# Kernel optimization log

Measured on AMD Instinct MI355X. Metric: run time of the kernel, lower is better.

The kernel has to match this reference:

```python
import jax, jax.numpy as jnp
import numpy as np

N, IN_C, E = 50000, 512, 800000
H, C = 2, 64          # heads, per-head channels
HC = H * C            # 128
OUT_C = 2
B = 64                # number of graphs
EPS = 1e-5
NEG_SLOPE = 0.2


def gat_conv(x, src, dst, W, a_src, a_dst, bias):
    """PyG GATConv (concat=True, add_self_loops already included in src/dst)."""
    n = x.shape[0]
    h = (x @ W).reshape(n, H, C)                      # [N,H,C]
    alpha_src = (h * a_src[None]).sum(-1)             # [N,H]
    alpha_dst = (h * a_dst[None]).sum(-1)             # [N,H]
    e = jax.nn.leaky_relu(alpha_src[src] + alpha_dst[dst], NEG_SLOPE)  # [E,H]
    # segment softmax over incoming edges of each destination node
    m = jax.ops.segment_max(e, dst, num_segments=n)   # [N,H]
    ex = jnp.exp(e - m[dst])
    denom = jax.ops.segment_sum(ex, dst, num_segments=n)
    alpha = ex / denom[dst]                           # [E,H]
    msg = h[src] * alpha[:, :, None]                  # [E,H,C]
    out = jax.ops.segment_sum(msg, dst, num_segments=n)  # [N,H,C]
    return out.reshape(n, HC) + bias


def batch_norm(x, gamma, beta):
    # BatchNorm1d in training mode: batch statistics over the node dim
    mu = x.mean(0)
    var = x.var(0)
    return gamma * (x - mu) * jax.lax.rsqrt(var + EPS) + beta


def setup_inputs() -> dict:
    key = jax.random.key(0)
    ks = jax.random.split(key, 16)
    x = jax.random.normal(ks[0], (N, IN_C), dtype=jnp.float32)
    edge_index = jax.random.randint(ks[1], (2, E), 0, N, dtype=jnp.int64)
    batch = jnp.sort(jax.random.randint(ks[2], (N,), 0, B, dtype=jnp.int64))
    g = lambda k, sh, fan: jax.random.normal(k, sh, dtype=jnp.float32) * (1.0 / np.sqrt(fan))
    return {
        "x": x, "edge_index": edge_index, "batch": batch,
        "W1": g(ks[3], (IN_C, HC), IN_C),
        "att_src1": g(ks[4], (H, C), C), "att_dst1": g(ks[5], (H, C), C),
        "b1": jnp.zeros((HC,), jnp.float32),
        "gamma1": jnp.ones((HC,), jnp.float32), "beta1": jnp.zeros((HC,), jnp.float32),
        "W2": g(ks[6], (HC, HC), HC),
        "att_src2": g(ks[7], (H, C), C), "att_dst2": g(ks[8], (H, C), C),
        "b2": jnp.zeros((HC,), jnp.float32),
        "gamma2": jnp.ones((HC,), jnp.float32), "beta2": jnp.zeros((HC,), jnp.float32),
        "Wlin": g(ks[9], (HC, OUT_C), HC),
        "blin": jnp.zeros((OUT_C,), jnp.float32),
    }


def reference(x, edge_index, batch, W1, att_src1, att_dst1, b1, gamma1, beta1,
              W2, att_src2, att_dst2, b2, gamma2, beta2, Wlin, blin):
    n = x.shape[0]
    # GATConv adds self-loops by default
    loop = jnp.arange(n, dtype=edge_index.dtype)
    src = jnp.concatenate([edge_index[0], loop])
    dst = jnp.concatenate([edge_index[1], loop])

    h = gat_conv(x, src, dst, W1, att_src1, att_dst1, b1)
    h = jax.nn.relu(batch_norm(h, gamma1, beta1))
    h = gat_conv(h, src, dst, W2, att_src2, att_dst2, b2)
    h = jax.nn.relu(batch_norm(h, gamma2, beta2))

    # global mean pool over graphs
    sums = jax.ops.segment_sum(h, batch, num_segments=B)           # [B,HC]
    cnt = jax.ops.segment_sum(jnp.ones((n,), h.dtype), batch, num_segments=B)
    pooled = sums / jnp.maximum(cnt, 1.0)[:, None]
    return pooled @ Wlin + blin                                    # [B,OUT_C]
```

## Files before the change

### kernel.cpp

```cpp
#include <hip/hip_runtime.h>
#include <hip/hip_bf16.h>
#include <cstdint>
#include <cstddef>

#define NN      50000
#define IN_C    512
#define EE      800000
#define ETOT    850000
#define HH      2
#define CC      64
#define HC      128
#define BB      64
#define OUTC    2
#define NEG_SLOPE 0.2f
#define BN_EPS  1e-5f

#define NBLK_SCAN ((NN + 255) / 256)

#define NXCD     8
#define NPX      ((NN + NXCD - 1) / NXCD)
#define EDGES_PER_SLOT 2048
#define NSLOT    ((ETOT + EDGES_PER_SLOT - 1) / EDGES_PER_SLOT)

typedef __bf16 bf16x8 __attribute__((ext_vector_type(8)));
typedef float  f32x4  __attribute__((ext_vector_type(4)));

__device__ __forceinline__ unsigned f2bf(float f) {
    __bf16 b = (__bf16)f;
    return (unsigned)__builtin_bit_cast(unsigned short, b);
}

__device__ __forceinline__ void gload_lds16(const float* g, float* l) {
    __builtin_amdgcn_global_load_lds(
        (const __attribute__((address_space(1))) unsigned*)g,
        (__attribute__((address_space(3))) unsigned*)l,
        16, 0, 0);
}

__global__ __launch_bounds__(256) void deg_kernel(const int* __restrict__ ei, int* __restrict__ deg)
{
    const int xcd  = blockIdx.x & (NXCD - 1);
    const int slot = blockIdx.x >> 3;
    const int lo = xcd * NPX, hi = lo + NPX;
    const int base = slot * EDGES_PER_SLOT;
#pragma unroll
    for (int it = 0; it < EDGES_PER_SLOT / 256; ++it) {
        int e = base + it * 256 + threadIdx.x;
        if (e < ETOT) {
            int d = (e < EE) ? ei[EE + e] : (e - EE);
            if (d >= lo && d < hi) atomicAdd(&deg[d], 1);
        }
    }
}

__global__ __launch_bounds__(256) void bsum_kernel(const int* __restrict__ deg, int* __restrict__ bsum)
{
    int i = blockIdx.x * 256 + threadIdx.x;
    int v = (i < NN) ? deg[i] : 0;
    int lane = threadIdx.x & 63, wv = threadIdx.x >> 6;
#pragma unroll
    for (int o = 32; o > 0; o >>= 1) v += __shfl_down(v, o);
    __shared__ int ws[4];
    if (lane == 0) ws[wv] = v;
    __syncthreads();
    if (threadIdx.x == 0) bsum[blockIdx.x] = ws[0] + ws[1] + ws[2] + ws[3];
}

__global__ __launch_bounds__(256) void bscan_kernel(
    const int* __restrict__ bsum, int* __restrict__ bofs, int* __restrict__ rowp)
{
    int t = threadIdx.x;
    int lane = t & 63, wv = t >> 6;
    int v = (t < NBLK_SCAN) ? bsum[t] : 0;
    int x = v;
#pragma unroll
    for (int o = 1; o < 64; o <<= 1) {
        int y = __shfl_up(x, o);
        if (lane >= o) x += y;
    }
    __shared__ int ws[4];
    if (lane == 63) ws[wv] = x;
    __syncthreads();
    int wo = 0;
#pragma unroll
    for (int w = 0; w < 4; ++w) if (w < wv) wo += ws[w];
    if (t < NBLK_SCAN) bofs[t] = x + wo - v;
    if (t == 0) rowp[NN] = ETOT;
}

__global__ __launch_bounds__(256) void bapply_kernel(
    const int* __restrict__ deg, const int* __restrict__ bofs,
    int* __restrict__ rowp, int* __restrict__ cur)
{
    int i = blockIdx.x * 256 + threadIdx.x;
    int v = (i < NN) ? deg[i] : 0;
    int lane = threadIdx.x & 63, wv = threadIdx.x >> 6;
    int x = v;
#pragma unroll
    for (int o = 1; o < 64; o <<= 1) {
        int y = __shfl_up(x, o);
        if (lane >= o) x += y;
    }
    __shared__ int ws[4];
    if (lane == 63) ws[wv] = x;
    __syncthreads();
    int wo = 0;
#pragma unroll
    for (int w = 0; w < 4; ++w) if (w < wv) wo += ws[w];
    if (i < NN) {
        int r = bofs[blockIdx.x] + x + wo - v;
        rowp[i] = r; cur[i] = r;
    }
}

__global__ __launch_bounds__(256) void scatter_kernel(
    const int* __restrict__ ei, int* __restrict__ cur, int* __restrict__ esrc)
{
    const int xcd  = blockIdx.x & (NXCD - 1);
    const int slot = blockIdx.x >> 3;
    const int lo = xcd * NPX, hi = lo + NPX;
    const int base = slot * EDGES_PER_SLOT;
#pragma unroll
    for (int it = 0; it < EDGES_PER_SLOT / 256; ++it) {
        int e = base + it * 256 + threadIdx.x;
        if (e < ETOT) {
            int s, d;
            if (e < EE) { s = ei[e]; d = ei[EE + e]; }
            else        { s = e - EE; d = s; }
            if (d >= lo && d < hi) {
                int pos = atomicAdd(&cur[d], 1);
                esrc[pos] = s;
            }
        }
    }
}

__global__ __launch_bounds__(256) void wfrag_kernel(
    const float* __restrict__ W1, unsigned short* __restrict__ Wf1,
    const float* __restrict__ W2, unsigned short* __restrict__ Wf2)
{
    int t = blockIdx.x * 256 + threadIdx.x;
    const float* W; unsigned short* Wf;
    if (t < IN_C * 16) { W = W1; Wf = Wf1; }
    else {
        t -= IN_C * 16;
        if (t >= HC * 16) return;
        W = W2; Wf = Wf2;
    }
    int lane = t & 63, frag = t >> 6;
    int kblk = frag >> 3, nt = frag & 7;
    int quad = lane >> 4, ln = lane & 15;
    int kbase = kblk * 32 + quad * 8;
    int n = nt * 16 + ln;
    unsigned short u[8];
#pragma unroll
    for (int j = 0; j < 8; ++j)
        u[j] = (unsigned short)f2bf(W[(size_t)(kbase + j) * HC + n]);
    ushort4 a; a.x = u[0]; a.y = u[1]; a.z = u[2]; a.w = u[3];
    ushort4 b; b.x = u[4]; b.y = u[5]; b.z = u[6]; b.w = u[7];
    *(ushort4*)(Wf + (size_t)t * 8)     = a;
    *(ushort4*)(Wf + (size_t)t * 8 + 4) = b;
}

template<int K, bool AFFINE>
__global__ __launch_bounds__(256) void mfma_gemm_kernel(
    const float* __restrict__ A, const unsigned short* __restrict__ Wf,
    const float* __restrict__ atts, const float* __restrict__ attd,
    unsigned* __restrict__ hb, float* __restrict__ as_, float* __restrict__ ad_,
    const float* __restrict__ sc, const float* __restrict__ sh)
{
    constexpr int NSTEP = K >> 5;
    __shared__ __align__(16) float Abuf[2][64 * 64];

    const int tid  = threadIdx.x;
    const int wave = tid >> 6, lane = tid & 63;
    const int quad = lane >> 4, ln = lane & 15;
    const int m0 = blockIdx.x * 64;

    const int srow = tid >> 3;
    const int g    = (tid & 7) ^ (srow & 7);
    int grow0 = m0 + srow;      if (grow0 > NN - 1) grow0 = NN - 1;
    int grow1 = m0 + srow + 32; if (grow1 > NN - 1) grow1 = NN - 1;
    const float* gsrc0 = A + (size_t)grow0 * K + g * 4;
    const float* gsrc1 = A + (size_t)grow1 * K + g * 4;

    const int rr = wave * 16 + ln;
    const int base_f = rr * 32;
    const int sA = (((quad * 2)     ^ (rr & 7)) * 4);
    const int sB = (((quad * 2 + 1) ^ (rr & 7)) * 4);

    const unsigned short* wbase = Wf + lane * 8;

    f32x4 acc[8];
#pragma unroll
    for (int nt = 0; nt < 8; ++nt) acc[nt] = (f32x4){0.f, 0.f, 0.f, 0.f};

    gload_lds16(gsrc0,      &Abuf[0][wave * 256]);
    gload_lds16(gsrc1,      &Abuf[0][1024 + wave * 256]);
    gload_lds16(gsrc0 + 32, &Abuf[0][2048 + wave * 256]);
    gload_lds16(gsrc1 + 32, &Abuf[0][3072 + wave * 256]);
    bf16x8 bfr[2][8];
#pragma unroll
    for (int nt = 0; nt < 8; ++nt) bfr[0][nt] = *(const bf16x8*)(wbase + nt * 512);

#pragma unroll
    for (int ks = 0; ks < NSTEP; ++ks) {
        const int sub  = ks & 1;
        const int cbuf = (ks >> 1) & 1;
        const int bsel = ks & 1;
        if (sub == 0) {
            __syncthreads();
            if (ks + 2 < NSTEP) {
                const float* n0 = gsrc0 + (size_t)(ks + 2) * 32;
                const float* n1 = gsrc1 + (size_t)(ks + 2) * 32;
                float* db = &Abuf[cbuf ^ 1][wave * 256];
                gload_lds16(n0,      db);
                gload_lds16(n1,      db + 1024);
                gload_lds16(n0 + 32, db + 2048);
                gload_lds16(n1 + 32, db + 3072);
            }
        }

        const float* fb_base = &Abuf[cbuf][sub * 2048 + base_f];
        float4 fa = *(const float4*)(fb_base + sA);
        float4 fb = *(const float4*)(fb_base + sB);
        float va[8] = {fa.x, fa.y, fa.z, fa.w, fb.x, fb.y, fb.z, fb.w};
        if (AFFINE) {
            const int kk = ks * 32 + quad * 8;
            const float4 s0 = *(const float4*)(sc + kk), s1 = *(const float4*)(sc + kk + 4);
            const float4 h0 = *(const float4*)(sh + kk), h1 = *(const float4*)(sh + kk + 4);
            va[0] = fmaxf(fmaf(s0.x, va[0], h0.x), 0.f);
            va[1] = fmaxf(fmaf(s0.y, va[1], h0.y), 0.f);
            va[2] = fmaxf(fmaf(s0.z, va[2], h0.z), 0.f);
            va[3] = fmaxf(fmaf(s0.w, va[3], h0.w), 0.f);
            va[4] = fmaxf(fmaf(s1.x, va[4], h1.x), 0.f);
            va[5] = fmaxf(fmaf(s1.y, va[5], h1.y), 0.f);
            va[6] = fmaxf(fmaf(s1.z, va[6], h1.z), 0.f);
            va[7] = fmaxf(fmaf(s1.w, va[7], h1.w), 0.f);
        }
        union { bf16x8 v; unsigned short u[8]; } af;
#pragma unroll
        for (int j = 0; j < 8; ++j) af.u[j] = (unsigned short)f2bf(va[j]);

        if (ks + 1 < NSTEP) {
            const unsigned short* wfp = wbase + (size_t)(ks + 1) * 4096;
#pragma unroll
            for (int nt = 0; nt < 8; ++nt)
                bfr[bsel ^ 1][nt] = *(const bf16x8*)(wfp + nt * 512);
        }

#pragma unroll
        for (int nt = 0; nt < 8; ++nt)
            acc[nt] = __builtin_amdgcn_mfma_f32_16x16x32_bf16(af.v, bfr[bsel][nt], acc[nt], 0, 0, 0);
    }

    float wsv[8], wdv[8];
#pragma unroll
    for (int nt = 0; nt < 8; ++nt) { wsv[nt] = atts[nt * 16 + ln]; wdv[nt] = attd[nt * 16 + ln]; }

    const int mbase = m0 + wave * 16 + quad * 4;
#pragma unroll
    for (int r = 0; r < 4; ++r) {
        int m = mbase + r;
        bool ok = (m < NN);
        float ps0 = 0.f, ps1 = 0.f, pd0 = 0.f, pd1 = 0.f;
#pragma unroll
        for (int nt = 0; nt < 8; ++nt) {
            float v = acc[nt][r];
            if (nt < 4) { ps0 = fmaf(v, wsv[nt], ps0); pd0 = fmaf(v, wdv[nt], pd0); }
            else        { ps1 = fmaf(v, wsv[nt], ps1); pd1 = fmaf(v, wdv[nt], pd1); }
        }
#pragma unroll
        for (int nt = 0; nt < 4; ++nt) {
            unsigned pk = f2bf(acc[nt][r]) | (f2bf(acc[nt + 4][r]) << 16);
            if (ok) hb[(size_t)m * 64 + nt * 16 + ln] = pk;
        }
#pragma unroll
        for (int o = 8; o > 0; o >>= 1) {
            ps0 += __shfl_down(ps0, o); ps1 += __shfl_down(ps1, o);
            pd0 += __shfl_down(pd0, o); pd1 += __shfl_down(pd1, o);
        }
        if (ok && ln == 0) {
            *(float2*)&as_[m * 2] = make_float2(ps0, ps1);
            *(float2*)&ad_[m * 2] = make_float2(pd0, pd1);
        }
    }
}

__global__ __launch_bounds__(256) void gat_agg_kernel(
    const int* __restrict__ rowp, const int* __restrict__ esrc,
    const float* __restrict__ as_, const float* __restrict__ ad_,
    const unsigned* __restrict__ hb, float* __restrict__ out,
    float* __restrict__ stats)
{
    const int tid  = threadIdx.x;
    const int node = (blockIdx.x * 256 + tid) >> 6;
    const int wave = tid >> 6;
    const int lane = tid & 63;
    int beg = rowp[node], end = rowp[node + 1];
    float2 adv = *(const float2*)&ad_[node * 2];

    float l0 = 0.f, l1 = 0.f, a0 = 0.f, a1 = 0.f;

    for (int j0 = beg; j0 < end; j0 += 64) {
        int nj = min(64, end - j0);
        int   sl  = 0;
        float p0l = 0.f, p1l = 0.f;
        if (j0 + lane < end) {
            sl = esrc[j0 + lane];
            float2 t = *(const float2*)&as_[sl * 2];
            float e0 = t.x + adv.x; e0 = fmaxf(e0, NEG_SLOPE * e0);
            float e1 = t.y + adv.y; e1 = fmaxf(e1, NEG_SLOPE * e1);
            p0l = __expf(e0); p1l = __expf(e1);
        }
        l0 += p0l; l1 += p1l;

        int j = 0;
        for (; j + 8 <= nj; j += 8) {
            int s0 = __shfl(sl, j),     s1 = __shfl(sl, j + 1);
            int s2 = __shfl(sl, j + 2), s3 = __shfl(sl, j + 3);
            int s4 = __shfl(sl, j + 4), s5 = __shfl(sl, j + 5);
            int s6 = __shfl(sl, j + 6), s7 = __shfl(sl, j + 7);
            unsigned u0 = hb[(size_t)s0 * 64 + lane];
            unsigned u1 = hb[(size_t)s1 * 64 + lane];
            unsigned u2 = hb[(size_t)s2 * 64 + lane];
            unsigned u3 = hb[(size_t)s3 * 64 + lane];
            unsigned u4 = hb[(size_t)s4 * 64 + lane];
            unsigned u5 = hb[(size_t)s5 * 64 + lane];
            unsigned u6 = hb[(size_t)s6 * 64 + lane];
            unsigned u7 = hb[(size_t)s7 * 64 + lane];
            a0 = fmaf(__shfl(p0l, j    ), __uint_as_float(u0 << 16), a0);
            a1 = fmaf(__shfl(p1l, j    ), __uint_as_float(u0 & 0xffff0000u), a1);
            a0 = fmaf(__shfl(p0l, j + 1), __uint_as_float(u1 << 16), a0);
            a1 = fmaf(__shfl(p1l, j + 1), __uint_as_float(u1 & 0xffff0000u), a1);
            a0 = fmaf(__shfl(p0l, j + 2), __uint_as_float(u2 << 16), a0);
            a1 = fmaf(__shfl(p1l, j + 2), __uint_as_float(u2 & 0xffff0000u), a1);
            a0 = fmaf(__shfl(p0l, j + 3), __uint_as_float(u3 << 16), a0);
            a1 = fmaf(__shfl(p1l, j + 3), __uint_as_float(u3 & 0xffff0000u), a1);
            a0 = fmaf(__shfl(p0l, j + 4), __uint_as_float(u4 << 16), a0);
            a1 = fmaf(__shfl(p1l, j + 4), __uint_as_float(u4 & 0xffff0000u), a1);
            a0 = fmaf(__shfl(p0l, j + 5), __uint_as_float(u5 << 16), a0);
            a1 = fmaf(__shfl(p1l, j + 5), __uint_as_float(u5 & 0xffff0000u), a1);
            a0 = fmaf(__shfl(p0l, j + 6), __uint_as_float(u6 << 16), a0);
            a1 = fmaf(__shfl(p1l, j + 6), __uint_as_float(u6 & 0xffff0000u), a1);
            a0 = fmaf(__shfl(p0l, j + 7), __uint_as_float(u7 << 16), a0);
            a1 = fmaf(__shfl(p1l, j + 7), __uint_as_float(u7 & 0xffff0000u), a1);
        }
        for (; j + 2 <= nj; j += 2) {
            int sA = __shfl(sl, j), sB = __shfl(sl, j + 1);
            unsigned uA = hb[(size_t)sA * 64 + lane];
            unsigned uB = hb[(size_t)sB * 64 + lane];
            a0 = fmaf(__shfl(p0l, j    ), __uint_as_float(uA << 16), a0);
            a1 = fmaf(__shfl(p1l, j    ), __uint_as_float(uA & 0xffff0000u), a1);
            a0 = fmaf(__shfl(p0l, j + 1), __uint_as_float(uB << 16), a0);
            a1 = fmaf(__shfl(p1l, j + 1), __uint_as_float(uB & 0xffff0000u), a1);
        }
        if (j < nj) {
            int s = __shfl(sl, j);
            unsigned u = hb[(size_t)s * 64 + lane];
            a0 = fmaf(__shfl(p0l, j), __uint_as_float(u << 16), a0);
            a1 = fmaf(__shfl(p1l, j), __uint_as_float(u & 0xffff0000u), a1);
        }
    }

#pragma unroll
    for (int o = 1; o < 64; o <<= 1) {
        l0 += __shfl_xor(l0, o); l1 += __shfl_xor(l1, o);
    }
    float v0 = a0 / l0;
    float v1 = a1 / l1;
    out[(size_t)node * HC + lane]      = v0;
    out[(size_t)node * HC + 64 + lane] = v1;

    __shared__ float red[4][256];
    red[wave][lane]      = v0;
    red[wave][64 + lane] = v1;
    __syncthreads();
    if (tid < 128) {
        float s = 0.f, q = 0.f;
#pragma unroll
        for (int w = 0; w < 4; ++w) {
            float v = red[w][tid];
            s += v; q = fmaf(v, v, q);
        }
        int slot = blockIdx.x & 63;
        atomicAdd(&stats[slot * 128 + tid], s);
        atomicAdd(&stats[64 * 128 + slot * 128 + tid], q);
    }
}

__global__ void bn_params_kernel(
    const float* __restrict__ stats, const float* __restrict__ gamma,
    const float* __restrict__ beta, float* __restrict__ sc, float* __restrict__ sh)
{
    int c = threadIdx.x;
    float su = 0.f, sq = 0.f;
#pragma unroll
    for (int k = 0; k < 64; ++k) {
        su += stats[k * 128 + c];
        sq += stats[64 * 128 + k * 128 + c];
    }
    const float inv_n = 1.0f / (float)NN;
    float mu = su * inv_n;
    float var = sq * inv_n - mu * mu;
    float rs = rsqrtf(var + BN_EPS);
    float s = gamma[c] * rs;
    sc[c] = s;
    sh[c] = beta[c] - mu * s;
}

__global__ __launch_bounds__(256) void pool_kernel(
    const float* __restrict__ x, const float* __restrict__ sc,
    const float* __restrict__ sh, const int* __restrict__ batch,
    float* __restrict__ pool, float* __restrict__ cnt)
{
    int c = threadIdx.x & 127;
    int half = threadIdx.x >> 7;
    int r0 = blockIdx.x * 64;
    int rend = min(r0 + 64, NN);
    float s = sc[c], b = sh[c];
    int cur = -1; float acc = 0.f, ccount = 0.f;
    for (int r = r0 + half; r < rend; r += 2) {
        int g = batch[r];
        if (g != cur) {
            if (cur >= 0) {
                atomicAdd(&pool[cur * HC + c], acc);
                if (c == 0) atomicAdd(&cnt[cur], ccount);
            }
            cur = g; acc = 0.f; ccount = 0.f;
        }
        float v = x[(size_t)r * HC + c];
        acc += fmaxf(fmaf(s, v, b), 0.f);
        ccount += 1.f;
    }
    if (cur >= 0) {
        atomicAdd(&pool[cur * HC + c], acc);
        if (c == 0) atomicAdd(&cnt[cur], ccount);
    }
}

__global__ void final_kernel(
    const float* __restrict__ pool, const float* __restrict__ cnt,
    const float* __restrict__ Wlin, const float* __restrict__ blin,
    float* __restrict__ outp)
{
    int t = threadIdx.x;
    int b = t >> 1, oc = t & 1;
    float inv = 1.f / fmaxf(cnt[b], 1.f);
    float s = blin[oc];
    for (int c = 0; c < HC; ++c)
        s += pool[b * HC + c] * inv * Wlin[c * 2 + oc];
    outp[b * 2 + oc] = s;
}

static constexpr size_t OFF_OUT   = 0;
static constexpr size_t OFF_AS    = OFF_OUT + (size_t)NN*HC;
static constexpr size_t OFF_AD    = OFF_AS  + (size_t)NN*HH;
static constexpr size_t OFF_ST1   = OFF_AD  + (size_t)NN*HH;
static constexpr size_t OFF_ST2   = OFF_ST1 + 2*64*128;
static constexpr size_t OFF_SC1   = OFF_ST2 + 2*64*128;
static constexpr size_t OFF_SH1   = OFF_SC1 + 128;
static constexpr size_t OFF_SC2   = OFF_SH1 + 128;
static constexpr size_t OFF_SH2   = OFF_SC2 + 128;
static constexpr size_t OFF_POOL  = OFF_SH2 + 128;
static constexpr size_t OFF_CNT   = OFF_POOL+ (size_t)BB*HC;
static constexpr size_t OFF_ZEND  = OFF_CNT + BB;
static constexpr size_t IOFF_DEG  = 0;
static constexpr size_t IOFF_ROWP = IOFF_DEG  + NN;
static constexpr size_t IOFF_CUR  = IOFF_ROWP + NN + 1;
static constexpr size_t IOFF_BSUM = IOFF_CUR  + NN;
static constexpr size_t IOFF_BOFS = IOFF_BSUM + NBLK_SCAN;
static constexpr size_t IOFF_ESRC = IOFF_BOFS + NBLK_SCAN;
static constexpr size_t IOFF_HB   = (IOFF_ESRC + ETOT + 3) & ~(size_t)3;
static constexpr size_t IOFF_WF1  = IOFF_HB + (size_t)NN*64;
static constexpr size_t IOFF_WF2  = IOFF_WF1 + (size_t)IN_C*64;
static constexpr size_t IOFF_END  = IOFF_WF2 + (size_t)HC*64;

extern "C" void kernel_launch(void* const* d_in, const int* in_sizes, int n_in,
                              void* d_out, int out_size, void* d_ws, size_t ws_size,
                              hipStream_t stream)
{
    const float* x       = (const float*)d_in[0];
    const int*   ei      = (const int*)  d_in[1];
    const int*   batch   = (const int*)  d_in[2];
    const float* W1      = (const float*)d_in[3];
    const float* atts1   = (const float*)d_in[4];
    const float* attd1   = (const float*)d_in[5];
    const float* gamma1  = (const float*)d_in[7];
    const float* beta1   = (const float*)d_in[8];
    const float* W2      = (const float*)d_in[9];
    const float* atts2   = (const float*)d_in[10];
    const float* attd2   = (const float*)d_in[11];
    const float* gamma2  = (const float*)d_in[13];
    const float* beta2   = (const float*)d_in[14];
    const float* Wlin    = (const float*)d_in[15];
    const float* blin    = (const float*)d_in[16];
    float* outp = (float*)d_out;

    float* ws    = (float*)d_ws;
    float* out   = ws + OFF_OUT;
    float* as_   = ws + OFF_AS;
    float* ad_   = ws + OFF_AD;
    float* st1   = ws + OFF_ST1;
    float* st2   = ws + OFF_ST2;
    float* sc1   = ws + OFF_SC1;
    float* sh1   = ws + OFF_SH1;
    float* sc2   = ws + OFF_SC2;
    float* sh2   = ws + OFF_SH2;
    float* pool  = ws + OFF_POOL;
    float* cnt   = ws + OFF_CNT;

    int* iws  = (int*)(ws + OFF_ZEND);
    int* deg  = iws + IOFF_DEG;
    int* rowp = iws + IOFF_ROWP;
    int* curp = iws + IOFF_CUR;
    int* bsum = iws + IOFF_BSUM;
    int* bofs = iws + IOFF_BOFS;
    int* esrc = iws + IOFF_ESRC;
    unsigned* hb = (unsigned*)(iws + IOFF_HB);
    unsigned short* Wf1 = (unsigned short*)(iws + IOFF_WF1);
    unsigned short* Wf2 = (unsigned short*)(iws + IOFF_WF2);

    const int BIN_BLK   = NXCD * NSLOT;
    const int GEMM_BLK  = (NN + 63) / 64;
    const int WAVE_BLK  = (NN + 3) / 4;
    const int POOL_BLK  = (NN + 63) / 64;
    const int WFRG_BLK  = (IN_C * 16 + HC * 16 + 255) / 256;

    hipMemsetAsync(st1, 0, (OFF_ZEND - OFF_ST1) * sizeof(float) + NN * sizeof(int), stream);

    wfrag_kernel<<<WFRG_BLK, 256, 0, stream>>>(W1, Wf1, W2, Wf2);
    deg_kernel<<<BIN_BLK, 256, 0, stream>>>(ei, deg);
    bsum_kernel<<<NBLK_SCAN, 256, 0, stream>>>(deg, bsum);
    bscan_kernel<<<1, 256, 0, stream>>>(bsum, bofs, rowp);
    bapply_kernel<<<NBLK_SCAN, 256, 0, stream>>>(deg, bofs, rowp, curp);
    scatter_kernel<<<BIN_BLK, 256, 0, stream>>>(ei, curp, esrc);

    mfma_gemm_kernel<IN_C, false><<<GEMM_BLK, 256, 0, stream>>>(
        x, Wf1, atts1, attd1, hb, as_, ad_, nullptr, nullptr);
    gat_agg_kernel<<<WAVE_BLK, 256, 0, stream>>>(rowp, esrc, as_, ad_, hb, out, st1);
    bn_params_kernel<<<1, 128, 0, stream>>>(st1, gamma1, beta1, sc1, sh1);

    mfma_gemm_kernel<HC, true><<<GEMM_BLK, 256, 0, stream>>>(
        out, Wf2, atts2, attd2, hb, as_, ad_, sc1, sh1);
    gat_agg_kernel<<<WAVE_BLK, 256, 0, stream>>>(rowp, esrc, as_, ad_, hb, out, st2);
    bn_params_kernel<<<1, 128, 0, stream>>>(st2, gamma2, beta2, sc2, sh2);

    pool_kernel<<<POOL_BLK, 256, 0, stream>>>(out, sc2, sh2, batch, pool, cnt);
    final_kernel<<<1, 128, 0, stream>>>(pool, cnt, Wlin, blin, outp);
}
```

Before: 418.9 us.

## Triple-buffer GEMM A tiles with vmcnt waits and deepen gather unroll

The MFMA GEMM moves from a double-buffered LDS pipeline with a __syncthreads per period to a three-slot ring. Tiles are prefetched two periods ahead, and explicit s_waitcnt vmcnt counts plus raw s_barrier let the weight loads stay in flight across barriers. Separately, the aggregation gather loop is unrolled from 8 to 16 outstanding row loads, with 4-wide and scalar tails, to raise memory-level parallelism. The larger LDS footprint (48KB per block) may reduce occupancy, and hand-tuned vmcnt values are fragile if the compiler reorders or changes the number of loads.

New measurement: 433.8 us. +3.5%, slower.

```diff
diff --git a/kernel.cpp b/kernel.cpp
--- a/kernel.cpp
+++ b/kernel.cpp
@@ -170,7 +170,8 @@
     const float* __restrict__ sc, const float* __restrict__ sh)
 {
     constexpr int NSTEP = K >> 5;
-    __shared__ __align__(16) float Abuf[2][64 * 64];
+    constexpr int NPER  = NSTEP >> 1;
+    __shared__ __align__(16) float Abuf[3][64 * 64];
 
     const int tid  = threadIdx.x;
     const int wave = tid >> 6, lane = tid & 63;
@@ -195,31 +196,34 @@
 #pragma unroll
     for (int nt = 0; nt < 8; ++nt) acc[nt] = (f32x4){0.f, 0.f, 0.f, 0.f};
 
-    gload_lds16(gsrc0,      &Abuf[0][wave * 256]);
-    gload_lds16(gsrc1,      &Abuf[0][1024 + wave * 256]);
-    gload_lds16(gsrc0 + 32, &Abuf[0][2048 + wave * 256]);
-    gload_lds16(gsrc1 + 32, &Abuf[0][3072 + wave * 256]);
+    auto STAGE = [&](int b, int p) {
+        const float* s0 = gsrc0 + (size_t)p * 64;
+        const float* s1 = gsrc1 + (size_t)p * 64;
+        float* db = &Abuf[b][wave * 256];
+        gload_lds16(s0,      db);
+        gload_lds16(s1,      db + 1024);
+        gload_lds16(s0 + 32, db + 2048);
+        gload_lds16(s1 + 32, db + 3072);
+    };
+
+    STAGE(0, 0);
+    STAGE(1, 1);
     bf16x8 bfr[2][8];
 #pragma unroll
     for (int nt = 0; nt < 8; ++nt) bfr[0][nt] = *(const bf16x8*)(wbase + nt * 512);
+    asm volatile("s_waitcnt vmcnt(0)" ::: "memory");
+    __builtin_amdgcn_sched_barrier(0);
+    __builtin_amdgcn_s_barrier();
+    __builtin_amdgcn_sched_barrier(0);
 
 #pragma unroll
     for (int ks = 0; ks < NSTEP; ++ks) {
+        const int per  = ks >> 1;
         const int sub  = ks & 1;
-        const int cbuf = (ks >> 1) & 1;
+        const int cbuf = per % 3;
         const int bsel = ks & 1;
-        if (sub == 0) {
-            __syncthreads();
-            if (ks + 2 < NSTEP) {
-                const float* n0 = gsrc0 + (size_t)(ks + 2) * 32;
-                const float* n1 = gsrc1 + (size_t)(ks + 2) * 32;
-                float* db = &Abuf[cbuf ^ 1][wave * 256];
-                gload_lds16(n0,      db);
-                gload_lds16(n1,      db + 1024);
-                gload_lds16(n0 + 32, db + 2048);
-                gload_lds16(n1 + 32, db + 3072);
-            }
-        }
+        if (sub == 0 && per + 2 < NPER)
+            STAGE((per + 2) % 3, per + 2);
 
         const float* fb_base = &Abuf[cbuf][sub * 2048 + base_f];
         float4 fa = *(const float4*)(fb_base + sA);
@@ -252,6 +256,14 @@
 #pragma unroll
         for (int nt = 0; nt < 8; ++nt)
             acc[nt] = __builtin_amdgcn_mfma_f32_16x16x32_bf16(af.v, bfr[bsel][nt], acc[nt], 0, 0, 0);
+
+        if (sub == 1 && ks + 1 < NSTEP) {
+            if (per + 2 < NPER) asm volatile("s_waitcnt vmcnt(20)" ::: "memory");
+            else                asm volatile("s_waitcnt vmcnt(16)" ::: "memory");
+            __builtin_amdgcn_sched_barrier(0);
+            __builtin_amdgcn_s_barrier();
+            __builtin_amdgcn_sched_barrier(0);
+        }
     }
 
     float wsv[8], wdv[8];
@@ -316,46 +328,33 @@
         l0 += p0l; l1 += p1l;
 
         int j = 0;
-        for (; j + 8 <= nj; j += 8) {
-            int s0 = __shfl(sl, j),     s1 = __shfl(sl, j + 1);
-            int s2 = __shfl(sl, j + 2), s3 = __shfl(sl, j + 3);
-            int s4 = __shfl(sl, j + 4), s5 = __shfl(sl, j + 5);
-            int s6 = __shfl(sl, j + 6), s7 = __shfl(sl, j + 7);
-            unsigned u0 = hb[(size_t)s0 * 64 + lane];
-            unsigned u1 = hb[(size_t)s1 * 64 + lane];
-            unsigned u2 = hb[(size_t)s2 * 64 + lane];
-            unsigned u3 = hb[(size_t)s3 * 64 + lane];
-            unsigned u4 = hb[(size_t)s4 * 64 + lane];
-            unsigned u5 = hb[(size_t)s5 * 64 + lane];
-            unsigned u6 = hb[(size_t)s6 * 64 + lane];
-            unsigned u7 = hb[(size_t)s7 * 64 + lane];
-            a0 = fmaf(__shfl(p0l, j    ), __uint_as_float(u0 << 16), a0);
-            a1 = fmaf(__shfl(p1l, j    ), __uint_as_float(u0 & 0xffff0000u), a1);
-            a0 = fmaf(__shfl(p0l, j + 1), __uint_as_float(u1 << 16), a0);
-            a1 = fmaf(__shfl(p1l, j + 1), __uint_as_float(u1 & 0xffff0000u), a1);
-            a0 = fmaf(__shfl(p0l, j + 2), __uint_as_float(u2 << 16), a0);
-            a1 = fmaf(__shfl(p1l, j + 2), __uint_as_float(u2 & 0xffff0000u), a1);
-            a0 = fmaf(__shfl(p0l, j + 3), __uint_as_float(u3 << 16), a0);
-            a1 = fmaf(__shfl(p1l, j + 3), __uint_as_float(u3 & 0xffff0000u), a1);
-            a0 = fmaf(__shfl(p0l, j + 4), __uint_as_float(u4 << 16), a0);
-            a1 = fmaf(__shfl(p1l, j + 4), __uint_as_float(u4 & 0xffff0000u), a1);
-            a0 = fmaf(__shfl(p0l, j + 5), __uint_as_float(u5 << 16), a0);
-            a1 = fmaf(__shfl(p1l, j + 5), __uint_as_float(u5 & 0xffff0000u), a1);
-            a0 = fmaf(__shfl(p0l, j + 6), __uint_as_float(u6 << 16), a0);
-            a1 = fmaf(__shfl(p1l, j + 6), __uint_as_float(u6 & 0xffff0000u), a1);
-            a0 = fmaf(__shfl(p0l, j + 7), __uint_as_float(u7 << 16), a0);
-            a1 = fmaf(__shfl(p1l, j + 7), __uint_as_float(u7 & 0xffff0000u), a1);
-        }
-        for (; j + 2 <= nj; j += 2) {
-            int sA = __shfl(sl, j), sB = __shfl(sl, j + 1);
-            unsigned uA = hb[(size_t)sA * 64 + lane];
-            unsigned uB = hb[(size_t)sB * 64 + lane];
-            a0 = fmaf(__shfl(p0l, j    ), __uint_as_float(uA << 16), a0);
-            a1 = fmaf(__shfl(p1l, j    ), __uint_as_float(uA & 0xffff0000u), a1);
-            a0 = fmaf(__shfl(p0l, j + 1), __uint_as_float(uB << 16), a0);
-            a1 = fmaf(__shfl(p1l, j + 1), __uint_as_float(uB & 0xffff0000u), a1);
-        }
-        if (j < nj) {
+        for (; j + 16 <= nj; j += 16) {
+            unsigned u[16];
+#pragma unroll
+            for (int q = 0; q < 16; ++q) {
+                int s = __shfl(sl, j + q);
+                u[q] = hb[(size_t)s * 64 + lane];
+            }
+#pragma unroll
+            for (int q = 0; q < 16; ++q) {
+                a0 = fmaf(__shfl(p0l, j + q), __uint_as_float(u[q] << 16), a0);
+                a1 = fmaf(__shfl(p1l, j + q), __uint_as_float(u[q] & 0xffff0000u), a1);
+            }
+        }
+        for (; j + 4 <= nj; j += 4) {
+            unsigned u[4];
+#pragma unroll
+            for (int q = 0; q < 4; ++q) {
+                int s = __shfl(sl, j + q);
+                u[q] = hb[(size_t)s * 64 + lane];
+            }
+#pragma unroll
+            for (int q = 0; q < 4; ++q) {
+                a0 = fmaf(__shfl(p0l, j + q), __uint_as_float(u[q] << 16), a0);
+                a1 = fmaf(__shfl(p1l, j + q), __uint_as_float(u[q] & 0xffff0000u), a1);
+            }
+        }
+        for (; j < nj; ++j) {
             int s = __shfl(sl, j);
             unsigned u = hb[(size_t)s * 64 + lane];
             a0 = fmaf(__shfl(p0l, j), __uint_as_float(u << 16), a0);
```
